# Optimization experiments

Hardware: AMD Instinct MI355X
Metric: run time of the kernel (lower is better)

## Reference

```python
import jax, jax.numpy as jnp
import numpy as np

D_TOK = 64
HID = 128


def _init_linear(key, fan_in, fan_out, bias_fill=None):
    kw, kb = jax.random.split(key)
    bound = 1.0 / np.sqrt(fan_in)
    W = jax.random.uniform(kw, (fan_in, fan_out), jnp.float32, -bound, bound)
    if bias_fill is None:
        b = jax.random.uniform(kb, (fan_out,), jnp.float32, -bound, bound)
    else:
        b = jnp.full((fan_out,), bias_fill, jnp.float32)
    return W, b


def setup_inputs() -> dict:
    key = jax.random.key(0)
    ks = jax.random.split(key, 7)
    N, E = 20000, 16
    tokens = jax.random.normal(ks[0], (N, E, D_TOK), jnp.float32)
    enc_W1, enc_b1 = _init_linear(ks[1], D_TOK, HID)
    enc_W2, enc_b2 = _init_linear(ks[2], HID, HID)
    spec_W1, spec_b1 = _init_linear(ks[3], 4 * HID, HID)
    spec_W2, spec_b2 = _init_linear(ks[4], HID, 1)
    def_W1, def_b1 = _init_linear(ks[5], 3 * HID, HID)
    def_W2, def_b2 = _init_linear(ks[6], HID, 1, bias_fill=-1.0)  # config.defer_bias
    return {
        "tokens": tokens,
        "enc_W1": enc_W1, "enc_b1": enc_b1, "enc_W2": enc_W2, "enc_b2": enc_b2,
        "spec_W1": spec_W1, "spec_b1": spec_b1, "spec_W2": spec_W2, "spec_b2": spec_b2,
        "def_W1": def_W1, "def_b1": def_b1, "def_W2": def_W2, "def_b2": def_b2,
        "full_index": 0,
        "top_k": 2,
    }


def _apply_top_k_mask(logits, full_index, top_k):
    # logits: [N, E]; mimic torch _apply_top_k_mask
    N, E = logits.shape
    if E <= 1:
        return logits
    neg = jnp.finfo(logits.dtype).min
    k = max(1, min(int(top_k), E - 1))
    masked = logits.at[:, full_index].set(neg)
    _, idx = jax.lax.top_k(masked, k)  # [N, k]
    rows = jnp.arange(N)[:, None]
    keep = jnp.zeros((N, E), bool).at[rows, idx].set(True)
    keep = keep.at[:, full_index].set(False)
    return jnp.where(keep, masked, neg)


def reference(tokens, enc_W1, enc_b1, enc_W2, enc_b2,
              spec_W1, spec_b1, spec_W2, spec_b2,
              def_W1, def_b1, def_W2, def_b2,
              full_index, top_k):
    neg = jnp.finfo(tokens.dtype).min
    # token encoder: two Linear+ReLU, applied per (row, expert)
    h = jax.nn.relu(tokens @ enc_W1 + enc_b1)
    encoded = jax.nn.relu(h @ enc_W2 + enc_b2)          # [N, E, H]
    full_token = encoded[:, full_index:full_index + 1]  # [N, 1, H]
    global_token = encoded.mean(axis=1, keepdims=True)  # [N, 1, H]
    token_delta = encoded - full_token
    global_delta = encoded - global_token
    pair = jnp.concatenate([encoded, token_delta, global_delta,
                            jnp.abs(token_delta)], axis=-1)  # [N, E, 4H]
    spec_h = jax.nn.relu(pair @ spec_W1 + spec_b1)
    specialist_logits = (spec_h @ spec_W2 + spec_b2)[..., 0]  # [N, E]
    specialist_logits = specialist_logits.at[:, full_index].set(neg)
    sparse_logits = _apply_top_k_mask(specialist_logits, full_index, top_k)
    w = jax.nn.softmax(sparse_logits, axis=1)
    w = w.at[:, full_index].set(0.0)
    mass = w.sum(axis=1, keepdims=True)
    w = jnp.where(mass > 0, w / jnp.maximum(mass, 1e-8), jnp.zeros_like(w))
    pooled = jnp.concatenate([full_token[:, 0], global_token[:, 0],
                              jnp.abs(token_delta).mean(axis=1)], axis=1)  # [N, 3H]
    def_h = jax.nn.relu(pooled @ def_W1 + def_b1)
    defer_prob = jax.nn.sigmoid(def_h @ def_W2 + def_b2)  # [N, 1]
    return w, defer_prob
```

## Files before the change

### kernel.cpp

```cpp
#include <hip/hip_runtime.h>
#include <math.h>

#define E 16
#define D 64
#define H 128
#define R 4

__global__ void wabc_prep(const float* __restrict__ specW1, float* __restrict__ wabc) {
    int i = blockIdx.x * blockDim.x + threadIdx.x;
    if (i < H * H) {
        wabc[i] = specW1[i] + specW1[H * H + i] + specW1[2 * H * H + i];
    }
}

template <bool USE_WABC>
__global__ __launch_bounds__(256, 2)
void router_kernel(const float* __restrict__ tokens,
                   const float* __restrict__ encW1, const float* __restrict__ encB1,
                   const float* __restrict__ encW2, const float* __restrict__ encB2,
                   const float* __restrict__ specW1, const float* __restrict__ specB1,
                   const float* __restrict__ specW2,
                   const float* __restrict__ defW1, const float* __restrict__ defB1,
                   const float* __restrict__ defW2, const float* __restrict__ defB2,
                   const int* __restrict__ fiPtr, const int* __restrict__ tkPtr,
                   const float* __restrict__ wabc,
                   float* __restrict__ out, int N) {
    __shared__ float buf[R * E * H];
    __shared__ float s_full[R * H];
    __shared__ float s_glob[R * H];
    __shared__ float s_mabs[R * H];

    const int tid  = threadIdx.x;
    const int lane = tid & 63;
    const int wq   = tid >> 6;
    const int n    = blockIdx.x * R + wq;
    if (n >= N) return;

    const int fi  = fiPtr[0];
    const int hw  = lane >> 5;
    const int jl  = lane & 31;
    const int jw0 = jl * 4;
    float* __restrict__ wbuf = buf + wq * (E * H);

    {
        const float4* __restrict__ src = (const float4*)(tokens + (size_t)n * (E * D));
        float4* dst = (float4*)wbuf;
#pragma unroll
        for (int it = 0; it < 4; it++) dst[lane + it * 64] = src[lane + it * 64];
    }
    __builtin_amdgcn_wave_barrier();

    {
        float acc[8][4];
#pragma unroll
        for (int m = 0; m < 8; m++)
#pragma unroll
            for (int j = 0; j < 4; j++) acc[m][j] = 0.f;
#pragma unroll 2
        for (int k = 0; k < D; k += 4) {
            float4 w0 = *(const float4*)(encW1 + (k + 0) * H + jw0);
            float4 w1 = *(const float4*)(encW1 + (k + 1) * H + jw0);
            float4 w2 = *(const float4*)(encW1 + (k + 2) * H + jw0);
            float4 w3 = *(const float4*)(encW1 + (k + 3) * H + jw0);
#pragma unroll
            for (int m = 0; m < 8; m++) {
                float4 t = *(const float4*)(wbuf + (hw * 8 + m) * D + k);
                acc[m][0] = fmaf(t.w, w3.x, fmaf(t.z, w2.x, fmaf(t.y, w1.x, fmaf(t.x, w0.x, acc[m][0]))));
                acc[m][1] = fmaf(t.w, w3.y, fmaf(t.z, w2.y, fmaf(t.y, w1.y, fmaf(t.x, w0.y, acc[m][1]))));
                acc[m][2] = fmaf(t.w, w3.z, fmaf(t.z, w2.z, fmaf(t.y, w1.z, fmaf(t.x, w0.z, acc[m][2]))));
                acc[m][3] = fmaf(t.w, w3.w, fmaf(t.z, w2.w, fmaf(t.y, w1.w, fmaf(t.x, w0.w, acc[m][3]))));
            }
        }
        float4 b = *(const float4*)(encB1 + jw0);
        __builtin_amdgcn_wave_barrier();
#pragma unroll
        for (int m = 0; m < 8; m++) {
            float4 o;
            o.x = fmaxf(acc[m][0] + b.x, 0.f);
            o.y = fmaxf(acc[m][1] + b.y, 0.f);
            o.z = fmaxf(acc[m][2] + b.z, 0.f);
            o.w = fmaxf(acc[m][3] + b.w, 0.f);
            *(float4*)(wbuf + (hw * 8 + m) * H + jw0) = o;
        }
    }
    __builtin_amdgcn_wave_barrier();

    {
        float acc[8][4];
#pragma unroll
        for (int m = 0; m < 8; m++)
#pragma unroll
            for (int j = 0; j < 4; j++) acc[m][j] = 0.f;
#pragma unroll 2
        for (int k = 0; k < H; k += 4) {
            float4 w0 = *(const float4*)(encW2 + (k + 0) * H + jw0);
            float4 w1 = *(const float4*)(encW2 + (k + 1) * H + jw0);
            float4 w2 = *(const float4*)(encW2 + (k + 2) * H + jw0);
            float4 w3 = *(const float4*)(encW2 + (k + 3) * H + jw0);
#pragma unroll
            for (int m = 0; m < 8; m++) {
                float4 t = *(const float4*)(wbuf + (hw * 8 + m) * H + k);
                acc[m][0] = fmaf(t.w, w3.x, fmaf(t.z, w2.x, fmaf(t.y, w1.x, fmaf(t.x, w0.x, acc[m][0]))));
                acc[m][1] = fmaf(t.w, w3.y, fmaf(t.z, w2.y, fmaf(t.y, w1.y, fmaf(t.x, w0.y, acc[m][1]))));
                acc[m][2] = fmaf(t.w, w3.z, fmaf(t.z, w2.z, fmaf(t.y, w1.z, fmaf(t.x, w0.z, acc[m][2]))));
                acc[m][3] = fmaf(t.w, w3.w, fmaf(t.z, w2.w, fmaf(t.y, w1.w, fmaf(t.x, w0.w, acc[m][3]))));
            }
        }
        float4 b = *(const float4*)(encB2 + jw0);
        __builtin_amdgcn_wave_barrier();
#pragma unroll
        for (int m = 0; m < 8; m++) {
            float4 o;
            o.x = fmaxf(acc[m][0] + b.x, 0.f);
            o.y = fmaxf(acc[m][1] + b.y, 0.f);
            o.z = fmaxf(acc[m][2] + b.z, 0.f);
            o.w = fmaxf(acc[m][3] + b.w, 0.f);
            *(float4*)(wbuf + (hw * 8 + m) * H + jw0) = o;
        }
    }
    __builtin_amdgcn_wave_barrier();

    {
        const int c2 = lane * 2;
        float2 fc = *(const float2*)(wbuf + fi * H + c2);
        float sx = 0.f, sy = 0.f, mx = 0.f, my = 0.f;
#pragma unroll
        for (int e = 0; e < E; e++) {
            float2 v = *(const float2*)(wbuf + e * H + c2);
            sx += v.x; sy += v.y;
            mx += fabsf(v.x - fc.x); my += fabsf(v.y - fc.y);
        }
        *(float2*)(s_full + wq * H + c2) = fc;
        *(float2*)(s_glob + wq * H + c2) = make_float2(sx * 0.0625f, sy * 0.0625f);
        *(float2*)(s_mabs + wq * H + c2) = make_float2(mx * 0.0625f, my * 0.0625f);
    }
    __builtin_amdgcn_wave_barrier();

    float4 biasr;
    {
        const float* __restrict__ Wb = specW1 + H * H;
        const float* __restrict__ Wc = specW1 + 2 * H * H;
        const int c0 = hw * 64;
        float accB[4] = {0.f, 0.f, 0.f, 0.f};
        float accD[4] = {0.f, 0.f, 0.f, 0.f};
#pragma unroll 2
        for (int cc = 0; cc < 64; cc++) {
            const int c = c0 + cc;
            float4 wb = *(const float4*)(Wb + c * H + jw0);
            float4 wc = *(const float4*)(Wc + c * H + jw0);
            float4 d0 = *(const float4*)(defW1 + c * H + jw0);
            float4 d1 = *(const float4*)(defW1 + (H + c) * H + jw0);
            float4 d2 = *(const float4*)(defW1 + (2 * H + c) * H + jw0);
            float fv = s_full[wq * H + c];
            float gv = s_glob[wq * H + c];
            float mv = s_mabs[wq * H + c];
            accB[0] = fmaf(gv, wc.x, fmaf(fv, wb.x, accB[0]));
            accB[1] = fmaf(gv, wc.y, fmaf(fv, wb.y, accB[1]));
            accB[2] = fmaf(gv, wc.z, fmaf(fv, wb.z, accB[2]));
            accB[3] = fmaf(gv, wc.w, fmaf(fv, wb.w, accB[3]));
            accD[0] = fmaf(mv, d2.x, fmaf(gv, d1.x, fmaf(fv, d0.x, accD[0])));
            accD[1] = fmaf(mv, d2.y, fmaf(gv, d1.y, fmaf(fv, d0.y, accD[1])));
            accD[2] = fmaf(mv, d2.z, fmaf(gv, d1.z, fmaf(fv, d0.z, accD[2])));
            accD[3] = fmaf(mv, d2.w, fmaf(gv, d1.w, fmaf(fv, d0.w, accD[3])));
        }
#pragma unroll
        for (int t = 0; t < 4; t++) {
            accB[t] += __shfl_xor(accB[t], 32, 64);
            accD[t] += __shfl_xor(accD[t], 32, 64);
        }
        float4 sb = *(const float4*)(specB1 + jw0);
        biasr = make_float4(sb.x - accB[0], sb.y - accB[1], sb.z - accB[2], sb.w - accB[3]);
        float4 db = *(const float4*)(defB1 + jw0);
        float4 dw = *(const float4*)(defW2 + jw0);
        float dv = fmaxf(db.x + accD[0], 0.f) * dw.x
                 + fmaxf(db.y + accD[1], 0.f) * dw.y
                 + fmaxf(db.z + accD[2], 0.f) * dw.z
                 + fmaxf(db.w + accD[3], 0.f) * dw.w;
#pragma unroll
        for (int off = 1; off < 32; off <<= 1) dv += __shfl_xor(dv, off, 64);
        if (lane == 0) {
            float s = dv + defB2[0];
            out[(size_t)N * E + n] = 1.f / (1.f + expf(-s));
        }
    }

    {
        float acc[8][4];
#pragma unroll
        for (int m = 0; m < 8; m++)
#pragma unroll
            for (int j = 0; j < 4; j++) acc[m][j] = 0.f;
        const float* __restrict__ Wd = specW1 + 3 * H * H;
        for (int k = 0; k < H; k += 4) {
            float4 wa0, wa1, wa2, wa3;
            if (USE_WABC) {
                wa0 = *(const float4*)(wabc + (k + 0) * H + jw0);
                wa1 = *(const float4*)(wabc + (k + 1) * H + jw0);
                wa2 = *(const float4*)(wabc + (k + 2) * H + jw0);
                wa3 = *(const float4*)(wabc + (k + 3) * H + jw0);
            } else {
#pragma unroll
                for (int t = 0; t < 4; t++) {
                    const float* p = specW1 + (k + t) * H + jw0;
                    float4 x0 = *(const float4*)(p);
                    float4 x1 = *(const float4*)(p + H * H);
                    float4 x2 = *(const float4*)(p + 2 * H * H);
                    float4 s4 = make_float4(x0.x + x1.x + x2.x, x0.y + x1.y + x2.y,
                                            x0.z + x1.z + x2.z, x0.w + x1.w + x2.w);
                    if (t == 0) wa0 = s4; else if (t == 1) wa1 = s4;
                    else if (t == 2) wa2 = s4; else wa3 = s4;
                }
            }
            float4 wd0 = *(const float4*)(Wd + (k + 0) * H + jw0);
            float4 wd1 = *(const float4*)(Wd + (k + 1) * H + jw0);
            float4 wd2 = *(const float4*)(Wd + (k + 2) * H + jw0);
            float4 wd3 = *(const float4*)(Wd + (k + 3) * H + jw0);
            float4 f4 = *(const float4*)(s_full + wq * H + k);
#pragma unroll
            for (int m = 0; m < 8; m++) {
                float4 ev = *(const float4*)(wbuf + (hw * 8 + m) * H + k);
                float ax = fabsf(ev.x - f4.x);
                float ay = fabsf(ev.y - f4.y);
                float az = fabsf(ev.z - f4.z);
                float aw = fabsf(ev.w - f4.w);
#pragma unroll
                for (int j = 0; j < 4; j++) {
                    const float* waj0 = &wa0.x, *waj1 = &wa1.x, *waj2 = &wa2.x, *waj3 = &wa3.x;
                    const float* wdj0 = &wd0.x, *wdj1 = &wd1.x, *wdj2 = &wd2.x, *wdj3 = &wd3.x;
                    float a = acc[m][j];
                    a = fmaf(ev.x, waj0[j], a);
                    a = fmaf(ev.y, waj1[j], a);
                    a = fmaf(ev.z, waj2[j], a);
                    a = fmaf(ev.w, waj3[j], a);
                    a = fmaf(ax, wdj0[j], a);
                    a = fmaf(ay, wdj1[j], a);
                    a = fmaf(az, wdj2[j], a);
                    a = fmaf(aw, wdj3[j], a);
                    acc[m][j] = a;
                }
            }
        }
        float4 w2 = *(const float4*)(specW2 + jw0);
        __builtin_amdgcn_wave_barrier();
#pragma unroll
        for (int m = 0; m < 8; m++) {
            float p = 0.f;
            p += fmaxf(acc[m][0] + biasr.x, 0.f) * w2.x;
            p += fmaxf(acc[m][1] + biasr.y, 0.f) * w2.y;
            p += fmaxf(acc[m][2] + biasr.z, 0.f) * w2.z;
            p += fmaxf(acc[m][3] + biasr.w, 0.f) * w2.w;
#pragma unroll
            for (int off = 1; off < 32; off <<= 1) p += __shfl_xor(p, off, 64);
            if (jl == 0) wbuf[hw * 8 + m] = p;
        }
    }
    __builtin_amdgcn_wave_barrier();

    if (lane == 0) {
        int k = tkPtr[0];
        if (k < 1) k = 1;
        if (k > E - 1) k = E - 1;
        unsigned chosen = 0u;
        for (int kk = 0; kk < k; kk++) {
            float bv = -INFINITY;
            int bi = 0;
            for (int e = 0; e < E; e++) {
                if (e == fi || ((chosen >> e) & 1u)) continue;
                float v = wbuf[e];
                if (v > bv) { bv = v; bi = e; }
            }
            chosen |= (1u << bi);
        }
        float mx = -INFINITY;
        for (int e = 0; e < E; e++)
            if ((chosen >> e) & 1u) { float v = wbuf[e]; if (v > mx) mx = v; }
        float ssum = 0.f;
        for (int e = 0; e < E; e++)
            if ((chosen >> e) & 1u) ssum += expf(wbuf[e] - mx);
        float inv = 1.f / ssum;
        for (int e = 0; e < E; e++) {
            float wv = 0.f;
            if ((chosen >> e) & 1u) wv = expf(wbuf[e] - mx) * inv;
            out[(size_t)n * E + e] = wv;
        }
    }
}

extern "C" void kernel_launch(void* const* d_in, const int* in_sizes, int n_in,
                              void* d_out, int out_size, void* d_ws, size_t ws_size,
                              hipStream_t stream) {
    (void)n_in; (void)out_size;
    const float* tokens = (const float*)d_in[0];
    const float* encW1  = (const float*)d_in[1];
    const float* encB1  = (const float*)d_in[2];
    const float* encW2  = (const float*)d_in[3];
    const float* encB2  = (const float*)d_in[4];
    const float* specW1 = (const float*)d_in[5];
    const float* specB1 = (const float*)d_in[6];
    const float* specW2 = (const float*)d_in[7];
    const float* defW1  = (const float*)d_in[9];
    const float* defB1  = (const float*)d_in[10];
    const float* defW2  = (const float*)d_in[11];
    const float* defB2  = (const float*)d_in[12];
    const int*   fiPtr  = (const int*)d_in[13];
    const int*   tkPtr  = (const int*)d_in[14];
    float* out = (float*)d_out;

    const int N = in_sizes[0] / (E * D);
    const int grid = (N + R - 1) / R;
    const bool useWs = (d_ws != nullptr) && (ws_size >= (size_t)(H * H * sizeof(float)));

    if (useWs) {
        wabc_prep<<<(H * H + 255) / 256, 256, 0, stream>>>(specW1, (float*)d_ws);
        router_kernel<true><<<grid, 256, 0, stream>>>(
            tokens, encW1, encB1, encW2, encB2, specW1, specB1, specW2,
            defW1, defB1, defW2, defB2, fiPtr, tkPtr, (const float*)d_ws, out, N);
    } else {
        router_kernel<false><<<grid, 256, 0, stream>>>(
            tokens, encW1, encB1, encW2, encB2, specW1, specB1, specW2,
            defW1, defB1, defW2, defB2, fiPtr, tkPtr, nullptr, out, N);
    }
}
```

Baseline: 717.8 us.

## Share pooled-feature GEMV weight loads across the block's four rows via LDS reduction

Result: faster. 698.7 us (-2.7%).

```diff
diff --git a/kernel.cpp b/kernel.cpp
--- a/kernel.cpp
+++ b/kernel.cpp
@@ -29,12 +29,13 @@
     __shared__ float s_full[R * H];
     __shared__ float s_glob[R * H];
     __shared__ float s_mabs[R * H];
+    __shared__ float s_part[R * R * H];
 
     const int tid  = threadIdx.x;
     const int lane = tid & 63;
     const int wq   = tid >> 6;
     const int n    = blockIdx.x * R + wq;
-    if (n >= N) return;
+    const bool active = (n < N);
 
     const int fi  = fiPtr[0];
     const int hw  = lane >> 5;
@@ -42,140 +43,201 @@
     const int jw0 = jl * 4;
     float* __restrict__ wbuf = buf + wq * (E * H);
 
-    {
-        const float4* __restrict__ src = (const float4*)(tokens + (size_t)n * (E * D));
-        float4* dst = (float4*)wbuf;
-#pragma unroll
-        for (int it = 0; it < 4; it++) dst[lane + it * 64] = src[lane + it * 64];
-    }
-    __builtin_amdgcn_wave_barrier();
-
-    {
-        float acc[8][4];
-#pragma unroll
-        for (int m = 0; m < 8; m++)
-#pragma unroll
-            for (int j = 0; j < 4; j++) acc[m][j] = 0.f;
+    if (active) {
+        {
+            const float4* __restrict__ src = (const float4*)(tokens + (size_t)n * (E * D));
+            float4* dst = (float4*)wbuf;
+#pragma unroll
+            for (int it = 0; it < 4; it++) dst[lane + it * 64] = src[lane + it * 64];
+        }
+        __builtin_amdgcn_wave_barrier();
+
+        {
+            float acc[8][4];
+#pragma unroll
+            for (int m = 0; m < 8; m++)
+#pragma unroll
+                for (int j = 0; j < 4; j++) acc[m][j] = 0.f;
 #pragma unroll 2
-        for (int k = 0; k < D; k += 4) {
-            float4 w0 = *(const float4*)(encW1 + (k + 0) * H + jw0);
-            float4 w1 = *(const float4*)(encW1 + (k + 1) * H + jw0);
-            float4 w2 = *(const float4*)(encW1 + (k + 2) * H + jw0);
-            float4 w3 = *(const float4*)(encW1 + (k + 3) * H + jw0);
+            for (int k = 0; k < D; k += 4) {
+                float4 w0 = *(const float4*)(encW1 + (k + 0) * H + jw0);
+                float4 w1 = *(const float4*)(encW1 + (k + 1) * H + jw0);
+                float4 w2 = *(const float4*)(encW1 + (k + 2) * H + jw0);
+                float4 w3 = *(const float4*)(encW1 + (k + 3) * H + jw0);
+#pragma unroll
+                for (int m = 0; m < 8; m++) {
+                    float4 t = *(const float4*)(wbuf + (hw * 8 + m) * D + k);
+                    acc[m][0] = fmaf(t.w, w3.x, fmaf(t.z, w2.x, fmaf(t.y, w1.x, fmaf(t.x, w0.x, acc[m][0]))));
+                    acc[m][1] = fmaf(t.w, w3.y, fmaf(t.z, w2.y, fmaf(t.y, w1.y, fmaf(t.x, w0.y, acc[m][1]))));
+                    acc[m][2] = fmaf(t.w, w3.z, fmaf(t.z, w2.z, fmaf(t.y, w1.z, fmaf(t.x, w0.z, acc[m][2]))));
+                    acc[m][3] = fmaf(t.w, w3.w, fmaf(t.z, w2.w, fmaf(t.y, w1.w, fmaf(t.x, w0.w, acc[m][3]))));
+                }
+            }
+            float4 b = *(const float4*)(encB1 + jw0);
+            __builtin_amdgcn_wave_barrier();
 #pragma unroll
             for (int m = 0; m < 8; m++) {
-                float4 t = *(const float4*)(wbuf + (hw * 8 + m) * D + k);
-                acc[m][0] = fmaf(t.w, w3.x, fmaf(t.z, w2.x, fmaf(t.y, w1.x, fmaf(t.x, w0.x, acc[m][0]))));
-                acc[m][1] = fmaf(t.w, w3.y, fmaf(t.z, w2.y, fmaf(t.y, w1.y, fmaf(t.x, w0.y, acc[m][1]))));
-                acc[m][2] = fmaf(t.w, w3.z, fmaf(t.z, w2.z, fmaf(t.y, w1.z, fmaf(t.x, w0.z, acc[m][2]))));
-                acc[m][3] = fmaf(t.w, w3.w, fmaf(t.z, w2.w, fmaf(t.y, w1.w, fmaf(t.x, w0.w, acc[m][3]))));
-            }
-        }
-        float4 b = *(const float4*)(encB1 + jw0);
+                float4 o;
+                o.x = fmaxf(acc[m][0] + b.x, 0.f);
+                o.y = fmaxf(acc[m][1] + b.y, 0.f);
+                o.z = fmaxf(acc[m][2] + b.z, 0.f);
+                o.w = fmaxf(acc[m][3] + b.w, 0.f);
+                *(float4*)(wbuf + (hw * 8 + m) * H + jw0) = o;
+            }
+        }
         __builtin_amdgcn_wave_barrier();
-#pragma unroll
-        for (int m = 0; m < 8; m++) {
-            float4 o;
-            o.x = fmaxf(acc[m][0] + b.x, 0.f);
-            o.y = fmaxf(acc[m][1] + b.y, 0.f);
-            o.z = fmaxf(acc[m][2] + b.z, 0.f);
-            o.w = fmaxf(acc[m][3] + b.w, 0.f);
-            *(float4*)(wbuf + (hw * 8 + m) * H + jw0) = o;
-        }
-    }
-    __builtin_amdgcn_wave_barrier();
-
-    {
-        float acc[8][4];
-#pragma unroll
-        for (int m = 0; m < 8; m++)
-#pragma unroll
-            for (int j = 0; j < 4; j++) acc[m][j] = 0.f;
+
+        {
+            float acc[8][4];
+#pragma unroll
+            for (int m = 0; m < 8; m++)
+#pragma unroll
+                for (int j = 0; j < 4; j++) acc[m][j] = 0.f;
 #pragma unroll 2
-        for (int k = 0; k < H; k += 4) {
-            float4 w0 = *(const float4*)(encW2 + (k + 0) * H + jw0);
-            float4 w1 = *(const float4*)(encW2 + (k + 1) * H + jw0);
-            float4 w2 = *(const float4*)(encW2 + (k + 2) * H + jw0);
-            float4 w3 = *(const float4*)(encW2 + (k + 3) * H + jw0);
+            for (int k = 0; k < H; k += 4) {
+                float4 w0 = *(const float4*)(encW2 + (k + 0) * H + jw0);
+                float4 w1 = *(const float4*)(encW2 + (k + 1) * H + jw0);
+                float4 w2 = *(const float4*)(encW2 + (k + 2) * H + jw0);
+                float4 w3 = *(const float4*)(encW2 + (k + 3) * H + jw0);
+#pragma unroll
+                for (int m = 0; m < 8; m++) {
+                    float4 t = *(const float4*)(wbuf + (hw * 8 + m) * H + k);
+                    acc[m][0] = fmaf(t.w, w3.x, fmaf(t.z, w2.x, fmaf(t.y, w1.x, fmaf(t.x, w0.x, acc[m][0]))));
+                    acc[m][1] = fmaf(t.w, w3.y, fmaf(t.z, w2.y, fmaf(t.y, w1.y, fmaf(t.x, w0.y, acc[m][1]))));
+                    acc[m][2] = fmaf(t.w, w3.z, fmaf(t.z, w2.z, fmaf(t.y, w1.z, fmaf(t.x, w0.z, acc[m][2]))));
+                    acc[m][3] = fmaf(t.w, w3.w, fmaf(t.z, w2.w, fmaf(t.y, w1.w, fmaf(t.x, w0.w, acc[m][3]))));
+                }
+            }
+            float4 b = *(const float4*)(encB2 + jw0);
+            __builtin_amdgcn_wave_barrier();
 #pragma unroll
             for (int m = 0; m < 8; m++) {
-                float4 t = *(const float4*)(wbuf + (hw * 8 + m) * H + k);
-                acc[m][0] = fmaf(t.w, w3.x, fmaf(t.z, w2.x, fmaf(t.y, w1.x, fmaf(t.x, w0.x, acc[m][0]))));
-                acc[m][1] = fmaf(t.w, w3.y, fmaf(t.z, w2.y, fmaf(t.y, w1.y, fmaf(t.x, w0.y, acc[m][1]))));
-                acc[m][2] = fmaf(t.w, w3.z, fmaf(t.z, w2.z, fmaf(t.y, w1.z, fmaf(t.x, w0.z, acc[m][2]))));
-                acc[m][3] = fmaf(t.w, w3.w, fmaf(t.z, w2.w, fmaf(t.y, w1.w, fmaf(t.x, w0.w, acc[m][3]))));
-            }
-        }
-        float4 b = *(const float4*)(encB2 + jw0);
+                float4 o;
+                o.x = fmaxf(acc[m][0] + b.x, 0.f);
+                o.y = fmaxf(acc[m][1] + b.y, 0.f);
+                o.z = fmaxf(acc[m][2] + b.z, 0.f);
+                o.w = fmaxf(acc[m][3] + b.w, 0.f);
+                *(float4*)(wbuf + (hw * 8 + m) * H + jw0) = o;
+            }
+        }
         __builtin_amdgcn_wave_barrier();
-#pragma unroll
-        for (int m = 0; m < 8; m++) {
-            float4 o;
-            o.x = fmaxf(acc[m][0] + b.x, 0.f);
-            o.y = fmaxf(acc[m][1] + b.y, 0.f);
-            o.z = fmaxf(acc[m][2] + b.z, 0.f);
-            o.w = fmaxf(acc[m][3] + b.w, 0.f);
-            *(float4*)(wbuf + (hw * 8 + m) * H + jw0) = o;
-        }
-    }
-    __builtin_amdgcn_wave_barrier();
-
-    {
-        const int c2 = lane * 2;
-        float2 fc = *(const float2*)(wbuf + fi * H + c2);
-        float sx = 0.f, sy = 0.f, mx = 0.f, my = 0.f;
-#pragma unroll
-        for (int e = 0; e < E; e++) {
-            float2 v = *(const float2*)(wbuf + e * H + c2);
-            sx += v.x; sy += v.y;
-            mx += fabsf(v.x - fc.x); my += fabsf(v.y - fc.y);
-        }
-        *(float2*)(s_full + wq * H + c2) = fc;
-        *(float2*)(s_glob + wq * H + c2) = make_float2(sx * 0.0625f, sy * 0.0625f);
-        *(float2*)(s_mabs + wq * H + c2) = make_float2(mx * 0.0625f, my * 0.0625f);
-    }
-    __builtin_amdgcn_wave_barrier();
-
-    float4 biasr;
+
+        {
+            const int c2 = lane * 2;
+            float2 fc = *(const float2*)(wbuf + fi * H + c2);
+            float sx = 0.f, sy = 0.f, mx = 0.f, my = 0.f;
+#pragma unroll
+            for (int e = 0; e < E; e++) {
+                float2 v = *(const float2*)(wbuf + e * H + c2);
+                sx += v.x; sy += v.y;
+                mx += fabsf(v.x - fc.x); my += fabsf(v.y - fc.y);
+            }
+            *(float2*)(s_full + wq * H + c2) = fc;
+            *(float2*)(s_glob + wq * H + c2) = make_float2(sx * 0.0625f, sy * 0.0625f);
+            *(float2*)(s_mabs + wq * H + c2) = make_float2(mx * 0.0625f, my * 0.0625f);
+        }
+    }
+    __syncthreads();
+
+    float accB[R][4];
+    float accD[R][4];
     {
         const float* __restrict__ Wb = specW1 + H * H;
         const float* __restrict__ Wc = specW1 + 2 * H * H;
-        const int c0 = hw * 64;
-        float accB[4] = {0.f, 0.f, 0.f, 0.f};
-        float accD[4] = {0.f, 0.f, 0.f, 0.f};
-#pragma unroll 2
-        for (int cc = 0; cc < 64; cc++) {
-            const int c = c0 + cc;
-            float4 wb = *(const float4*)(Wb + c * H + jw0);
-            float4 wc = *(const float4*)(Wc + c * H + jw0);
-            float4 d0 = *(const float4*)(defW1 + c * H + jw0);
-            float4 d1 = *(const float4*)(defW1 + (H + c) * H + jw0);
-            float4 d2 = *(const float4*)(defW1 + (2 * H + c) * H + jw0);
-            float fv = s_full[wq * H + c];
-            float gv = s_glob[wq * H + c];
-            float mv = s_mabs[wq * H + c];
-            accB[0] = fmaf(gv, wc.x, fmaf(fv, wb.x, accB[0]));
-            accB[1] = fmaf(gv, wc.y, fmaf(fv, wb.y, accB[1]));
-            accB[2] = fmaf(gv, wc.z, fmaf(fv, wb.z, accB[2]));
-            accB[3] = fmaf(gv, wc.w, fmaf(fv, wb.w, accB[3]));
-            accD[0] = fmaf(mv, d2.x, fmaf(gv, d1.x, fmaf(fv, d0.x, accD[0])));
-            accD[1] = fmaf(mv, d2.y, fmaf(gv, d1.y, fmaf(fv, d0.y, accD[1])));
-            accD[2] = fmaf(mv, d2.z, fmaf(gv, d1.z, fmaf(fv, d0.z, accD[2])));
-            accD[3] = fmaf(mv, d2.w, fmaf(gv, d1.w, fmaf(fv, d0.w, accD[3])));
-        }
-#pragma unroll
-        for (int t = 0; t < 4; t++) {
-            accB[t] += __shfl_xor(accB[t], 32, 64);
-            accD[t] += __shfl_xor(accD[t], 32, 64);
-        }
+        const int cbase = wq * 32 + hw * 16;
+#pragma unroll
+        for (int r = 0; r < R; r++)
+#pragma unroll
+            for (int j = 0; j < 4; j++) { accB[r][j] = 0.f; accD[r][j] = 0.f; }
+        for (int c4 = 0; c4 < 4; c4++) {
+            float4 fv4[R], gv4[R], mv4[R];
+#pragma unroll
+            for (int r = 0; r < R; r++) {
+                fv4[r] = *(const float4*)(s_full + r * H + cbase + c4 * 4);
+                gv4[r] = *(const float4*)(s_glob + r * H + cbase + c4 * 4);
+                mv4[r] = *(const float4*)(s_mabs + r * H + cbase + c4 * 4);
+            }
+#pragma unroll
+            for (int cc = 0; cc < 4; cc++) {
+                const int c = cbase + c4 * 4 + cc;
+                float4 wb = *(const float4*)(Wb + c * H + jw0);
+                float4 wc = *(const float4*)(Wc + c * H + jw0);
+                float4 d0 = *(const float4*)(defW1 + c * H + jw0);
+                float4 d1 = *(const float4*)(defW1 + (H + c) * H + jw0);
+                float4 d2 = *(const float4*)(defW1 + (2 * H + c) * H + jw0);
+#pragma unroll
+                for (int r = 0; r < R; r++) {
+                    const float fv = (&fv4[r].x)[cc];
+                    const float gv = (&gv4[r].x)[cc];
+                    const float mv = (&mv4[r].x)[cc];
+                    accB[r][0] = fmaf(gv, wc.x, fmaf(fv, wb.x, accB[r][0]));
+                    accB[r][1] = fmaf(gv, wc.y, fmaf(fv, wb.y, accB[r][1]));
+                    accB[r][2] = fmaf(gv, wc.z, fmaf(fv, wb.z, accB[r][2]));
+                    accB[r][3] = fmaf(gv, wc.w, fmaf(fv, wb.w, accB[r][3]));
+                    accD[r][0] = fmaf(mv, d2.x, fmaf(gv, d1.x, fmaf(fv, d0.x, accD[r][0])));
+                    accD[r][1] = fmaf(mv, d2.y, fmaf(gv, d1.y, fmaf(fv, d0.y, accD[r][1])));
+                    accD[r][2] = fmaf(mv, d2.z, fmaf(gv, d1.z, fmaf(fv, d0.z, accD[r][2])));
+                    accD[r][3] = fmaf(mv, d2.w, fmaf(gv, d1.w, fmaf(fv, d0.w, accD[r][3])));
+                }
+            }
+        }
+#pragma unroll
+        for (int r = 0; r < R; r++)
+#pragma unroll
+            for (int j = 0; j < 4; j++) {
+                accB[r][j] += __shfl_xor(accB[r][j], 32, 64);
+                accD[r][j] += __shfl_xor(accD[r][j], 32, 64);
+            }
+#pragma unroll
+        for (int rr = 0; rr < 2; rr++) {
+            const int r = hw * 2 + rr;
+            *(float4*)(s_part + (wq * R + r) * H + jw0) =
+                make_float4(accB[r][0], accB[r][1], accB[r][2], accB[r][3]);
+        }
+    }
+    __syncthreads();
+
+    float4 biasr;
+    {
+        float4 p0 = *(const float4*)(s_part + (0 * R + wq) * H + jw0);
+        float4 p1 = *(const float4*)(s_part + (1 * R + wq) * H + jw0);
+        float4 p2 = *(const float4*)(s_part + (2 * R + wq) * H + jw0);
+        float4 p3 = *(const float4*)(s_part + (3 * R + wq) * H + jw0);
         float4 sb = *(const float4*)(specB1 + jw0);
-        biasr = make_float4(sb.x - accB[0], sb.y - accB[1], sb.z - accB[2], sb.w - accB[3]);
+        biasr.x = sb.x - (((p0.x + p1.x) + p2.x) + p3.x);
+        biasr.y = sb.y - (((p0.y + p1.y) + p2.y) + p3.y);
+        biasr.z = sb.z - (((p0.z + p1.z) + p2.z) + p3.z);
+        biasr.w = sb.w - (((p0.w + p1.w) + p2.w) + p3.w);
+    }
+    __syncthreads();
+
+    {
+#pragma unroll
+        for (int rr = 0; rr < 2; rr++) {
+            const int r = hw * 2 + rr;
+            *(float4*)(s_part + (wq * R + r) * H + jw0) =
+                make_float4(accD[r][0], accD[r][1], accD[r][2], accD[r][3]);
+        }
+    }
+    __syncthreads();
+
+    if (!active) return;
+
+    {
+        float4 q0 = *(const float4*)(s_part + (0 * R + wq) * H + jw0);
+        float4 q1 = *(const float4*)(s_part + (1 * R + wq) * H + jw0);
+        float4 q2 = *(const float4*)(s_part + (2 * R + wq) * H + jw0);
+        float4 q3 = *(const float4*)(s_part + (3 * R + wq) * H + jw0);
         float4 db = *(const float4*)(defB1 + jw0);
         float4 dw = *(const float4*)(defW2 + jw0);
-        float dv = fmaxf(db.x + accD[0], 0.f) * dw.x
-                 + fmaxf(db.y + accD[1], 0.f) * dw.y
-                 + fmaxf(db.z + accD[2], 0.f) * dw.z
-                 + fmaxf(db.w + accD[3], 0.f) * dw.w;
+        float pd0 = db.x + (((q0.x + q1.x) + q2.x) + q3.x);
+        float pd1 = db.y + (((q0.y + q1.y) + q2.y) + q3.y);
+        float pd2 = db.z + (((q0.z + q1.z) + q2.z) + q3.z);
+        float pd3 = db.w + (((q0.w + q1.w) + q2.w) + q3.w);
+        float dv = fmaxf(pd0, 0.f) * dw.x
+                 + fmaxf(pd1, 0.f) * dw.y
+                 + fmaxf(pd2, 0.f) * dw.z
+                 + fmaxf(pd3, 0.f) * dw.w;
 #pragma unroll
         for (int off = 1; off < 32; off <<= 1) dv += __shfl_xor(dv, off, 64);
         if (lane == 0) {
```
